# Kernel tuning notes

Measured on AMD Instinct MI355X. Metric: run time of the kernel, lower is better.

The kernel has to match this reference:

```python
import jax, jax.numpy as jnp
import numpy as np

N_HEAD = 16


def setup_inputs() -> dict:
    key = jax.random.key(0)
    k1, k2, k3 = jax.random.split(key, 3)
    B, T, C = 2, 2048, 1024
    x = jax.random.normal(k1, (B, T, C), dtype=jnp.float32)
    Wqkv = jax.random.normal(k2, (C, 3 * C), dtype=jnp.float32) * 0.02
    bqkv = jnp.zeros((3 * C,), dtype=jnp.float32)
    Wproj = jax.random.normal(k3, (C, C), dtype=jnp.float32) * 0.02
    bproj = jnp.zeros((C,), dtype=jnp.float32)
    return {"x": x, "Wqkv": Wqkv, "bqkv": bqkv, "Wproj": Wproj, "bproj": bproj}


def reference(x, Wqkv, bqkv, Wproj, bproj):
    b, t, c = x.shape
    h = N_HEAD
    d = c // h  # head_dim
    # qkv projection, split into q,k,v per head: (b,t,3,h,d)
    qkv = (x @ Wqkv + bqkv).reshape(b, t, 3, h, d)
    q, k, v = qkv[:, :, 0], qkv[:, :, 1], qkv[:, :, 2]  # each (b,t,h,d)
    # Faithful quirk of original: n_state = head_dim // heads, scale = 1/sqrt(n_state)
    scale = jnp.float32(1.0 / np.sqrt(d // h))
    # attn_mode == 'all': dense non-causal attention
    w = jnp.einsum('bqhd,bkhd->bhqk', q, k)  # (b,h,t,t)
    w = jax.nn.softmax(w * scale, axis=-1)
    a = jnp.einsum('bhqk,bkhd->bqhd', w, v).reshape(b, t, c)
    return a @ Wproj + bproj
```

## Files before the change

### kernel.cpp

```cpp
#include <hip/hip_runtime.h>

typedef float floatx4 __attribute__((ext_vector_type(4)));
typedef __bf16 bf16x8 __attribute__((ext_vector_type(8)));
typedef __bf16 bf16x4 __attribute__((ext_vector_type(4)));
typedef short short4v __attribute__((ext_vector_type(4)));

#define MFMA16 __builtin_amdgcn_mfma_f32_16x16x32_bf16

static __device__ __forceinline__ short4v b2s(bf16x4 x) {
  union { bf16x4 b; short4v s; } u; u.b = x; return u.s;
}
#define MFMAPV(a, b, c) \
  __builtin_amdgcn_mfma_f32_16x16x16bf16_1k(b2s(a), b2s(b), (c), 0, 0, 0)

typedef const __attribute__((address_space(1))) void* gas_t;
typedef __attribute__((address_space(3))) void* las_t;
#define GLD16(g, l) __builtin_amdgcn_global_load_lds((gas_t)(g), (las_t)(l), 16, 0, 0)

static __device__ __forceinline__ unsigned short f2bf(float f) {
  union { float f; unsigned int u; } v; v.f = f;
  unsigned int r = v.u + 0x7fffu + ((v.u >> 16) & 1u);
  return (unsigned short)(r >> 16);
}

static __device__ __forceinline__ void cast_transpose_tile(
    const float* __restrict__ in, unsigned short* __restrict__ out,
    int R, int C, int bx, int by) {
  const int r0 = by * 64, c0 = bx * 64;
  const int tid = threadIdx.x;
  __shared__ float tl[64][65];
  const int rr = tid >> 4, cc = (tid & 15) * 4;
#pragma unroll
  for (int i = 0; i < 4; ++i) {
    int row = rr + i * 16;
    float4 v = *(const float4*)(in + (size_t)(r0 + row) * C + c0 + cc);
    tl[row][cc] = v.x; tl[row][cc + 1] = v.y;
    tl[row][cc + 2] = v.z; tl[row][cc + 3] = v.w;
  }
  __syncthreads();
  const int cl = tid >> 2, rbase = (tid & 3) * 16;
  unsigned short o[16];
#pragma unroll
  for (int j = 0; j < 16; ++j) o[j] = f2bf(tl[rbase + j][cl]);
  unsigned short* dst = out + (size_t)(c0 + cl) * R + r0 + rbase;
  *(uint4*)dst = *(uint4*)o;
  *(uint4*)(dst + 8) = *(uint4*)(o + 8);
}

__global__ __launch_bounds__(256) void prologue_kernel(
    const float* __restrict__ x, unsigned short* __restrict__ Xb,
    const float* __restrict__ Wqkv, unsigned short* __restrict__ Wqkvt,
    const float* __restrict__ Wproj, unsigned short* __restrict__ Wprojt) {
  const int bid = blockIdx.x;
  if (bid < 4096) {
    int i = bid * 256 + threadIdx.x;
    float4 v = ((const float4*)x)[i];
    ushort4 o;
    o.x = f2bf(v.x); o.y = f2bf(v.y); o.z = f2bf(v.z); o.w = f2bf(v.w);
    ((ushort4*)Xb)[i] = o;
  } else if (bid < 4096 + 768) {
    int b2 = bid - 4096;
    cast_transpose_tile(Wqkv, Wqkvt, 1024, 3072, b2 % 48, b2 / 48);
  } else {
    int b3 = bid - 4096 - 768;
    cast_transpose_tile(Wproj, Wprojt, 1024, 1024, b3 % 16, b3 / 16);
  }
}

__global__ __launch_bounds__(256) void gemm_qkv(
    const unsigned short* __restrict__ A,
    const unsigned short* __restrict__ Bt,
    const float* __restrict__ bias,
    unsigned short* __restrict__ Q,
    unsigned short* __restrict__ Kc,
    unsigned short* __restrict__ Vt) {
  const int K = 1024;
  const int m0 = blockIdx.y * 128, n0 = blockIdx.x * 128;
  const int tid = threadIdx.x, w = tid >> 6, l = tid & 63;
  const int l16 = l & 15, lq = l >> 4;
  const int wm = w >> 1, wn = w & 1;
  const int which = n0 >> 10;

  __shared__ __align__(16) unsigned short SH[16384];
  unsigned short* As = SH;
  unsigned short* Bs = SH + 8192;

  floatx4 acc[4][4] = {};

  int sA[4], sB[4];
  unsigned ldso[4];
#pragma unroll
  for (int j = 0; j < 4; ++j) {
    int s = j * 256 + tid;
    int row = s >> 3, blk = (s & 7) ^ (row & 7);
    sA[j] = (m0 + row) * K + blk * 8;
    sB[j] = (n0 + row) * K + blk * 8;
    ldso[j] = (unsigned)(j * 256 + w * 64) * 8;
  }

  if (which == 2) {
    for (int k0 = 0; k0 < K; k0 += 64) {
      __syncthreads();
#pragma unroll
      for (int j = 0; j < 4; ++j) {
        GLD16(A + sA[j] + k0, As + ldso[j]);
        GLD16(Bt + sB[j] + k0, Bs + ldso[j]);
      }
      __syncthreads();
#pragma unroll
      for (int kk = 0; kk < 2; ++kk) {
        bf16x8 af[4], bf[4];
#pragma unroll
        for (int mi = 0; mi < 4; ++mi) {
          int row = wm * 64 + mi * 16 + l16;
          int blk = (kk * 4 + lq) ^ (l16 & 7);
          af[mi] = *(const bf16x8*)(As + row * 64 + blk * 8);
        }
#pragma unroll
        for (int ni = 0; ni < 4; ++ni) {
          int row = wn * 64 + ni * 16 + l16;
          int blk = (kk * 4 + lq) ^ (l16 & 7);
          bf[ni] = *(const bf16x8*)(Bs + row * 64 + blk * 8);
        }
#pragma unroll
        for (int ni = 0; ni < 4; ++ni)
#pragma unroll
          for (int mi = 0; mi < 4; ++mi)
            acc[mi][ni] = MFMA16(af[mi], bf[ni], acc[mi][ni], 0, 0, 0);
      }
    }
    float bv[4];
#pragma unroll
    for (int ni = 0; ni < 4; ++ni) bv[ni] = bias[n0 + wn * 64 + ni * 16 + l16];
    __syncthreads();
    unsigned short* E = SH + w * 2304;
    const int bh = (m0 >> 11) * 16 + ((n0 & 1023) >> 6) + wn;
    const int tt0 = (m0 & 2047) + wm * 64;
#pragma unroll
    for (int p = 0; p < 2; ++p) {
#pragma unroll
      for (int n2 = 0; n2 < 2; ++n2) {
        int ni = p * 2 + n2;
#pragma unroll
        for (int mi = 0; mi < 4; ++mi) {
          floatx4 vv = acc[mi][ni] + bv[ni];
          *(bf16x4*)(E + (n2 * 16 + l16) * 72 + mi * 16 + lq * 4) =
              __builtin_convertvector(vv, bf16x4);
        }
      }
#pragma unroll
      for (int s = 0; s < 4; ++s) {
        int dl = s * 8 + (l >> 3);
        bf16x8 vv = *(const bf16x8*)(E + dl * 72 + (l & 7) * 8);
        *(bf16x8*)(Vt + ((size_t)bh * 64 + p * 32 + dl) * 2048 + tt0 +
                   (l & 7) * 8) = vv;
      }
    }
  } else {
    for (int k0 = 0; k0 < K; k0 += 64) {
      __syncthreads();
#pragma unroll
      for (int j = 0; j < 4; ++j) {
        GLD16(A + sA[j] + k0, As + ldso[j]);
        GLD16(Bt + sB[j] + k0, Bs + ldso[j]);
      }
      __syncthreads();
#pragma unroll
      for (int kk = 0; kk < 2; ++kk) {
        bf16x8 af[4], bf[4];
#pragma unroll
        for (int mi = 0; mi < 4; ++mi) {
          int row = wm * 64 + mi * 16 + l16;
          int blk = (kk * 4 + lq) ^ (l16 & 7);
          af[mi] = *(const bf16x8*)(As + row * 64 + blk * 8);
        }
#pragma unroll
        for (int ni = 0; ni < 4; ++ni) {
          int row = wn * 64 + ni * 16 + l16;
          int blk = (kk * 4 + lq) ^ (l16 & 7);
          bf[ni] = *(const bf16x8*)(Bs + row * 64 + blk * 8);
        }
#pragma unroll
        for (int ni = 0; ni < 4; ++ni)
#pragma unroll
          for (int mi = 0; mi < 4; ++mi)
            acc[mi][ni] = MFMA16(bf[ni], af[mi], acc[mi][ni], 0, 0, 0);
      }
    }
    const float sc = (which == 0) ? 0.7213475204444817f : 1.0f;
    unsigned short* dst = (which == 0) ? Q : Kc;
    __syncthreads();
    unsigned short* E = SH + w * 2304;
    const int bh = (m0 >> 11) * 16 + ((n0 & 1023) >> 6) + wn;
    const size_t gbase = ((size_t)bh * 2048 + (m0 & 2047) + wm * 64) * 64;
#pragma unroll
    for (int p = 0; p < 2; ++p) {
#pragma unroll
      for (int m2 = 0; m2 < 2; ++m2) {
        int mi = p * 2 + m2;
#pragma unroll
        for (int ni = 0; ni < 4; ++ni) {
          int col0 = n0 + wn * 64 + ni * 16 + lq * 4;
          floatx4 bv = *(const floatx4*)(bias + col0);
          floatx4 vv = (acc[mi][ni] + bv) * sc;
          *(bf16x4*)(E + (m2 * 16 + l16) * 72 + ni * 16 + lq * 4) =
              __builtin_convertvector(vv, bf16x4);
        }
      }
#pragma unroll
      for (int s = 0; s < 4; ++s) {
        int rl = s * 8 + (l >> 3);
        bf16x8 vv = *(const bf16x8*)(E + rl * 72 + (l & 7) * 8);
        *(bf16x8*)(dst + gbase + (size_t)(p * 32 + rl) * 64 + (l & 7) * 8) =
            vv;
      }
    }
  }
}

__global__ __launch_bounds__(256, 2) void attn_kernel(
    const unsigned short* __restrict__ Q,
    const unsigned short* __restrict__ Kc,
    const unsigned short* __restrict__ Vt,
    unsigned short* __restrict__ AO) {
  const int T = 2048;
  const int bh = blockIdx.y, q0 = blockIdx.x * 128;
  const int tid = threadIdx.x, w = tid >> 6, l = tid & 63;
  const int l16 = l & 15, lq = l >> 4;
  const int kh = w >> 1, wq = w & 1;
  const int h128 = tid & 127;

  __shared__ __align__(16) unsigned short KVs[2][2][2][4096];
  __shared__ __align__(16) float Lred[512];

  bf16x8 qf[4][2];
  {
    const unsigned short* qb = Q + ((size_t)bh * T + q0 + wq * 64) * 64;
#pragma unroll
    for (int qs = 0; qs < 4; ++qs) {
      const unsigned short* qr = qb + (qs * 16 + l16) * 64;
      qf[qs][0] = *(const bf16x8*)(qr + lq * 8);
      qf[qs][1] = *(const bf16x8*)(qr + 32 + lq * 8);
    }
  }

  float l_lane[4] = {0.f, 0.f, 0.f, 0.f};
  floatx4 o_acc[4][4] = {};

  const unsigned short* kbase = Kc + (size_t)bh * T * 64;
  const unsigned short* vbase = Vt + (size_t)bh * 64 * T;
  int kro[4], vro[4];
  unsigned ldso[4];
#pragma unroll
  for (int j = 0; j < 4; ++j) {
    int s = j * 128 + h128;
    int row = s >> 3, blk = (s & 7) ^ (row & 7);
    kro[j] = row * 64 + blk * 8;
    vro[j] = row * T + blk * 8;
    ldso[j] = (unsigned)(j * 128 + wq * 64) * 8;
  }

  const int swz0 = (0 + lq) ^ (l16 & 7);
  const int swz1 = (4 + lq) ^ (l16 & 7);

  {
    int c0 = kh * 16;
#pragma unroll
    for (int j = 0; j < 4; ++j) {
      GLD16(kbase + c0 * 4096 + kro[j], &KVs[0][kh][0][ldso[j]]);
      GLD16(vbase + c0 * 64 + vro[j], &KVs[1][kh][0][ldso[j]]);
    }
  }

  for (int it = 0; it < 16; ++it) {
    __syncthreads();
    if (it + 1 < 16) {
      int cn = kh * 16 + it + 1, nb = (it + 1) & 1;
#pragma unroll
      for (int j = 0; j < 4; ++j) {
        GLD16(kbase + cn * 4096 + kro[j], &KVs[0][kh][nb][ldso[j]]);
        GLD16(vbase + cn * 64 + vro[j], &KVs[1][kh][nb][ldso[j]]);
      }
    }
    const unsigned short* kb = KVs[0][kh][it & 1];
    const unsigned short* vb = KVs[1][kh][it & 1];

    bf16x8 kf[4][2];
#pragma unroll
    for (int ct = 0; ct < 4; ++ct) {
      const unsigned short* kr = kb + (ct * 16 + l16) * 64;
      kf[ct][0] = *(const bf16x8*)(kr + swz0 * 8);
      kf[ct][1] = *(const bf16x8*)(kr + swz1 * 8);
    }

    bf16x4 pf[4][4];
#pragma unroll
    for (int qs = 0; qs < 4; ++qs) {
      floatx4 st[4];
#pragma unroll
      for (int ct = 0; ct < 4; ++ct) {
        floatx4 z = {};
        z = MFMA16(kf[ct][0], qf[qs][0], z, 0, 0, 0);
        z = MFMA16(kf[ct][1], qf[qs][1], z, 0, 0, 0);
        st[ct] = z;
      }
#pragma unroll
      for (int ct = 0; ct < 4; ++ct) {
        floatx4 pv;
        pv[0] = __builtin_amdgcn_exp2f(st[ct][0]);
        pv[1] = __builtin_amdgcn_exp2f(st[ct][1]);
        pv[2] = __builtin_amdgcn_exp2f(st[ct][2]);
        pv[3] = __builtin_amdgcn_exp2f(st[ct][3]);
        l_lane[qs] += (pv[0] + pv[1]) + (pv[2] + pv[3]);
        pf[qs][ct] = __builtin_convertvector(pv, bf16x4);
      }
    }

    const int vs = l16 & 7;
#pragma unroll
    for (int dt = 0; dt < 4; ++dt) {
      const unsigned short* vr = vb + (dt * 16 + l16) * 64 + (lq & 1) * 4;
      bf16x4 vf[4];
#pragma unroll
      for (int ct = 0; ct < 4; ++ct)
        vf[ct] = *(const bf16x4*)(vr + (((2 * ct + (lq >> 1)) ^ vs) << 3));
#pragma unroll
      for (int qs = 0; qs < 4; ++qs)
#pragma unroll
        for (int ct = 0; ct < 4; ++ct)
          o_acc[dt][qs] = MFMAPV(vf[ct], pf[qs][ct], o_acc[dt][qs]);
    }
  }

  __syncthreads();
  float* ex = (float*)&KVs[0][0][0][0];
  if (kh == 1) {
    float* r = ex + wq * 4096;
#pragma unroll
    for (int dt = 0; dt < 4; ++dt)
#pragma unroll
      for (int qs = 0; qs < 4; ++qs)
        *(floatx4*)(r + ((dt * 4 + qs) * 64 + l) * 4) = o_acc[dt][qs];
#pragma unroll
    for (int qs = 0; qs < 4; ++qs) Lred[(wq * 4 + qs) * 64 + l] = l_lane[qs];
  }
  __syncthreads();
  if (kh == 0) {
    const float* r = ex + wq * 4096;
    const int b = bh >> 4, h = bh & 15;
#pragma unroll
    for (int qs = 0; qs < 4; ++qs) {
      float ls = l_lane[qs] + Lred[(wq * 4 + qs) * 64 + l];
      ls += __shfl_xor(ls, 16, 64);
      ls += __shfl_xor(ls, 32, 64);
      float inv = 1.0f / ls;
      int t = q0 + wq * 64 + qs * 16 + l16;
#pragma unroll
      for (int dt = 0; dt < 4; ++dt) {
        floatx4 ov = o_acc[dt][qs] +
                     *(const floatx4*)(r + ((dt * 4 + qs) * 64 + l) * 4);
        ov *= inv;
        bf16x4 ob = __builtin_convertvector(ov, bf16x4);
        *(bf16x4*)(AO + ((size_t)b * 2048 + t) * 1024 + h * 64 + dt * 16 +
                   lq * 4) = ob;
      }
    }
  }
}

__global__ __launch_bounds__(256) void gemm_proj(
    const unsigned short* __restrict__ A,
    const unsigned short* __restrict__ Bt,
    const float* __restrict__ bias,
    float* __restrict__ out) {
  const int K = 1024, N = 1024;
  const int m0 = blockIdx.y * 128, n0 = blockIdx.x * 64;
  const int tid = threadIdx.x, w = tid >> 6, l = tid & 63;
  const int l16 = l & 15, lq = l >> 4;

  __shared__ __align__(16) unsigned short As[128 * 64];
  __shared__ __align__(16) unsigned short Bs[64 * 64];

  floatx4 acc[2][4] = {};

  int sA[4], sB[2];
  unsigned ldsoA[4], ldsoB[2];
#pragma unroll
  for (int j = 0; j < 4; ++j) {
    int s = j * 256 + tid;
    int row = s >> 3, blk = (s & 7) ^ (row & 7);
    sA[j] = (m0 + row) * K + blk * 8;
    ldsoA[j] = (unsigned)(j * 256 + w * 64) * 8;
  }
#pragma unroll
  for (int j = 0; j < 2; ++j) {
    int s = j * 256 + tid;
    int row = s >> 3, blk = (s & 7) ^ (row & 7);
    sB[j] = (n0 + row) * K + blk * 8;
    ldsoB[j] = (unsigned)(j * 256 + w * 64) * 8;
  }

  for (int k0 = 0; k0 < K; k0 += 64) {
    __syncthreads();
#pragma unroll
    for (int j = 0; j < 4; ++j) GLD16(A + sA[j] + k0, As + ldsoA[j]);
#pragma unroll
    for (int j = 0; j < 2; ++j) GLD16(Bt + sB[j] + k0, Bs + ldsoB[j]);
    __syncthreads();
#pragma unroll
    for (int kk = 0; kk < 2; ++kk) {
      bf16x8 af[2], bf[4];
#pragma unroll
      for (int mi = 0; mi < 2; ++mi) {
        int row = w * 32 + mi * 16 + l16;
        int blk = (kk * 4 + lq) ^ (l16 & 7);
        af[mi] = *(const bf16x8*)(As + row * 64 + blk * 8);
      }
#pragma unroll
      for (int ni = 0; ni < 4; ++ni) {
        int row = ni * 16 + l16;
        int blk = (kk * 4 + lq) ^ (l16 & 7);
        bf[ni] = *(const bf16x8*)(Bs + row * 64 + blk * 8);
      }
#pragma unroll
      for (int ni = 0; ni < 4; ++ni)
#pragma unroll
        for (int mi = 0; mi < 2; ++mi)
          acc[mi][ni] = MFMA16(bf[ni], af[mi], acc[mi][ni], 0, 0, 0);
    }
  }

#pragma unroll
  for (int mi = 0; mi < 2; ++mi) {
    int t = m0 + w * 32 + mi * 16 + l16;
#pragma unroll
    for (int ni = 0; ni < 4; ++ni) {
      int col0 = n0 + ni * 16 + lq * 4;
      floatx4 bv = *(const floatx4*)(bias + col0);
      *(floatx4*)(out + (size_t)t * N + col0) = acc[mi][ni] + bv;
    }
  }
}

extern "C" void kernel_launch(void* const* d_in, const int* in_sizes, int n_in,
                              void* d_out, int out_size, void* d_ws,
                              size_t ws_size, hipStream_t stream) {
  const float* x     = (const float*)d_in[0];
  const float* Wqkv  = (const float*)d_in[1];
  const float* bqkv  = (const float*)d_in[2];
  const float* Wproj = (const float*)d_in[3];
  const float* bproj = (const float*)d_in[4];
  float* out = (float*)d_out;

  unsigned short* Xb     = (unsigned short*)d_ws;
  unsigned short* Wqkvt  = Xb + 4194304;
  unsigned short* Wprojt = Wqkvt + 3145728;
  unsigned short* Qb     = Wprojt + 1048576;
  unsigned short* Kb     = Qb + 4194304;
  unsigned short* Vtb    = Kb + 4194304;
  unsigned short* AOb    = Vtb + 4194304;

  prologue_kernel<<<5120, 256, 0, stream>>>(x, Xb, Wqkv, Wqkvt, Wproj, Wprojt);
  gemm_qkv<<<dim3(24, 32), 256, 0, stream>>>(Xb, Wqkvt, bqkv, Qb, Kb, Vtb);
  attn_kernel<<<dim3(16, 32), 256, 0, stream>>>(Qb, Kb, Vtb, AOb);
  gemm_proj<<<dim3(16, 32), 256, 0, stream>>>(AOb, Wprojt, bproj, out);
}
```

Before: 184.9 us.

## Rewrite attention kernel with 32x32x16 MFMA and no intra-block KV split

The attention kernel now uses 32x32x16 bf16 MFMAs for both QK^T and PV. Each wave owns 32 query rows and walks all 32 key chunks, so the two-half KV split and its LDS reduction at the end are removed. The P fragments are repacked across lanes with xor-32 shuffles so they can feed the PV MFMA directly. The cost is more sequential iterations per block and fewer independent accumulators per wave, with shuffle overhead added inside the inner loop.

```diff
diff --git a/kernel.cpp b/kernel.cpp
--- a/kernel.cpp
+++ b/kernel.cpp
@@ -1,17 +1,14 @@
 #include <hip/hip_runtime.h>
 
 typedef float floatx4 __attribute__((ext_vector_type(4)));
+typedef float floatx16 __attribute__((ext_vector_type(16)));
 typedef __bf16 bf16x8 __attribute__((ext_vector_type(8)));
 typedef __bf16 bf16x4 __attribute__((ext_vector_type(4)));
-typedef short short4v __attribute__((ext_vector_type(4)));
+typedef __bf16 bf16x2 __attribute__((ext_vector_type(2)));
+typedef float floatx2 __attribute__((ext_vector_type(2)));
 
 #define MFMA16 __builtin_amdgcn_mfma_f32_16x16x32_bf16
-
-static __device__ __forceinline__ short4v b2s(bf16x4 x) {
-  union { bf16x4 b; short4v s; } u; u.b = x; return u.s;
-}
-#define MFMAPV(a, b, c) \
-  __builtin_amdgcn_mfma_f32_16x16x16bf16_1k(b2s(a), b2s(b), (c), 0, 0, 0)
+#define MFMA32 __builtin_amdgcn_mfma_f32_32x32x16_bf16
 
 typedef const __attribute__((address_space(1))) void* gas_t;
 typedef __attribute__((address_space(3))) void* las_t;
@@ -21,6 +18,13 @@
   union { float f; unsigned int u; } v; v.f = f;
   unsigned int r = v.u + 0x7fffu + ((v.u >> 16) & 1u);
   return (unsigned short)(r >> 16);
+}
+
+static __device__ __forceinline__ unsigned pk2(float a, float b) {
+  floatx2 v; v[0] = a; v[1] = b;
+  union { bf16x2 h; unsigned u; } u;
+  u.h = __builtin_convertvector(v, bf16x2);
+  return u.u;
 }
 
 static __device__ __forceinline__ void cast_transpose_tile(
@@ -226,146 +230,123 @@
   const int T = 2048;
   const int bh = blockIdx.y, q0 = blockIdx.x * 128;
   const int tid = threadIdx.x, w = tid >> 6, l = tid & 63;
-  const int l16 = l & 15, lq = l >> 4;
-  const int kh = w >> 1, wq = w & 1;
-  const int h128 = tid & 127;
-
-  __shared__ __align__(16) unsigned short KVs[2][2][2][4096];
-  __shared__ __align__(16) float Lred[512];
-
-  bf16x8 qf[4][2];
+  const int r31 = l & 31, g = l >> 5;
+
+  __shared__ __align__(16) unsigned short KVs[2][2][4096];
+
+  bf16x8 qf[4];
   {
-    const unsigned short* qb = Q + ((size_t)bh * T + q0 + wq * 64) * 64;
-#pragma unroll
-    for (int qs = 0; qs < 4; ++qs) {
-      const unsigned short* qr = qb + (qs * 16 + l16) * 64;
-      qf[qs][0] = *(const bf16x8*)(qr + lq * 8);
-      qf[qs][1] = *(const bf16x8*)(qr + 32 + lq * 8);
-    }
-  }
-
-  float l_lane[4] = {0.f, 0.f, 0.f, 0.f};
-  floatx4 o_acc[4][4] = {};
+    const unsigned short* qr =
+        Q + ((size_t)bh * T + q0 + w * 32 + r31) * 64 + g * 8;
+#pragma unroll
+    for (int ds = 0; ds < 4; ++ds) qf[ds] = *(const bf16x8*)(qr + ds * 16);
+  }
+
+  floatx16 o_acc[2] = {};
+  float l_lane = 0.f;
 
   const unsigned short* kbase = Kc + (size_t)bh * T * 64;
   const unsigned short* vbase = Vt + (size_t)bh * 64 * T;
-  int kro[4], vro[4];
-  unsigned ldso[4];
-#pragma unroll
-  for (int j = 0; j < 4; ++j) {
-    int s = j * 128 + h128;
+  int kro[2], vro[2];
+  unsigned ldso[2];
+#pragma unroll
+  for (int j = 0; j < 2; ++j) {
+    int s = j * 256 + tid;
     int row = s >> 3, blk = (s & 7) ^ (row & 7);
     kro[j] = row * 64 + blk * 8;
     vro[j] = row * T + blk * 8;
-    ldso[j] = (unsigned)(j * 128 + wq * 64) * 8;
-  }
-
-  const int swz0 = (0 + lq) ^ (l16 & 7);
-  const int swz1 = (4 + lq) ^ (l16 & 7);
-
-  {
-    int c0 = kh * 16;
-#pragma unroll
-    for (int j = 0; j < 4; ++j) {
-      GLD16(kbase + c0 * 4096 + kro[j], &KVs[0][kh][0][ldso[j]]);
-      GLD16(vbase + c0 * 64 + vro[j], &KVs[1][kh][0][ldso[j]]);
-    }
-  }
-
-  for (int it = 0; it < 16; ++it) {
+    ldso[j] = (unsigned)(j * 256 + (tid & 192)) * 8;
+  }
+
+#pragma unroll
+  for (int j = 0; j < 2; ++j) {
+    GLD16(kbase + kro[j], &KVs[0][0][ldso[j]]);
+    GLD16(vbase + vro[j], &KVs[0][1][ldso[j]]);
+  }
+
+  for (int c = 0; c < 32; ++c) {
     __syncthreads();
-    if (it + 1 < 16) {
-      int cn = kh * 16 + it + 1, nb = (it + 1) & 1;
-#pragma unroll
-      for (int j = 0; j < 4; ++j) {
-        GLD16(kbase + cn * 4096 + kro[j], &KVs[0][kh][nb][ldso[j]]);
-        GLD16(vbase + cn * 64 + vro[j], &KVs[1][kh][nb][ldso[j]]);
-      }
-    }
-    const unsigned short* kb = KVs[0][kh][it & 1];
-    const unsigned short* vb = KVs[1][kh][it & 1];
-
-    bf16x8 kf[4][2];
-#pragma unroll
-    for (int ct = 0; ct < 4; ++ct) {
-      const unsigned short* kr = kb + (ct * 16 + l16) * 64;
-      kf[ct][0] = *(const bf16x8*)(kr + swz0 * 8);
-      kf[ct][1] = *(const bf16x8*)(kr + swz1 * 8);
-    }
-
-    bf16x4 pf[4][4];
-#pragma unroll
-    for (int qs = 0; qs < 4; ++qs) {
-      floatx4 st[4];
-#pragma unroll
-      for (int ct = 0; ct < 4; ++ct) {
-        floatx4 z = {};
-        z = MFMA16(kf[ct][0], qf[qs][0], z, 0, 0, 0);
-        z = MFMA16(kf[ct][1], qf[qs][1], z, 0, 0, 0);
-        st[ct] = z;
-      }
-#pragma unroll
-      for (int ct = 0; ct < 4; ++ct) {
-        floatx4 pv;
-        pv[0] = __builtin_amdgcn_exp2f(st[ct][0]);
-        pv[1] = __builtin_amdgcn_exp2f(st[ct][1]);
-        pv[2] = __builtin_amdgcn_exp2f(st[ct][2]);
-        pv[3] = __builtin_amdgcn_exp2f(st[ct][3]);
-        l_lane[qs] += (pv[0] + pv[1]) + (pv[2] + pv[3]);
-        pf[qs][ct] = __builtin_convertvector(pv, bf16x4);
-      }
-    }
-
-    const int vs = l16 & 7;
-#pragma unroll
-    for (int dt = 0; dt < 4; ++dt) {
-      const unsigned short* vr = vb + (dt * 16 + l16) * 64 + (lq & 1) * 4;
-      bf16x4 vf[4];
-#pragma unroll
-      for (int ct = 0; ct < 4; ++ct)
-        vf[ct] = *(const bf16x4*)(vr + (((2 * ct + (lq >> 1)) ^ vs) << 3));
-#pragma unroll
-      for (int qs = 0; qs < 4; ++qs)
-#pragma unroll
-        for (int ct = 0; ct < 4; ++ct)
-          o_acc[dt][qs] = MFMAPV(vf[ct], pf[qs][ct], o_acc[dt][qs]);
-    }
-  }
-
-  __syncthreads();
-  float* ex = (float*)&KVs[0][0][0][0];
-  if (kh == 1) {
-    float* r = ex + wq * 4096;
-#pragma unroll
-    for (int dt = 0; dt < 4; ++dt)
-#pragma unroll
-      for (int qs = 0; qs < 4; ++qs)
-        *(floatx4*)(r + ((dt * 4 + qs) * 64 + l) * 4) = o_acc[dt][qs];
-#pragma unroll
-    for (int qs = 0; qs < 4; ++qs) Lred[(wq * 4 + qs) * 64 + l] = l_lane[qs];
-  }
-  __syncthreads();
-  if (kh == 0) {
-    const float* r = ex + wq * 4096;
-    const int b = bh >> 4, h = bh & 15;
-#pragma unroll
-    for (int qs = 0; qs < 4; ++qs) {
-      float ls = l_lane[qs] + Lred[(wq * 4 + qs) * 64 + l];
-      ls += __shfl_xor(ls, 16, 64);
-      ls += __shfl_xor(ls, 32, 64);
-      float inv = 1.0f / ls;
-      int t = q0 + wq * 64 + qs * 16 + l16;
-#pragma unroll
-      for (int dt = 0; dt < 4; ++dt) {
-        floatx4 ov = o_acc[dt][qs] +
-                     *(const floatx4*)(r + ((dt * 4 + qs) * 64 + l) * 4);
-        ov *= inv;
-        bf16x4 ob = __builtin_convertvector(ov, bf16x4);
-        *(bf16x4*)(AO + ((size_t)b * 2048 + t) * 1024 + h * 64 + dt * 16 +
-                   lq * 4) = ob;
-      }
-    }
-  }
+    if (c < 31) {
+      const int nb = (c + 1) & 1;
+#pragma unroll
+      for (int j = 0; j < 2; ++j) {
+        GLD16(kbase + (c + 1) * 4096 + kro[j], &KVs[nb][0][ldso[j]]);
+        GLD16(vbase + (c + 1) * 64 + vro[j], &KVs[nb][1][ldso[j]]);
+      }
+    }
+    const unsigned short* kb = KVs[c & 1][0];
+    const unsigned short* vb = KVs[c & 1][1];
+
+    floatx16 sac[2];
+#pragma unroll
+    for (int kt = 0; kt < 2; ++kt) {
+      const int row = kt * 32 + r31, rx = row & 7;
+      const unsigned short* kr = kb + row * 64;
+      floatx16 z = {};
+#pragma unroll
+      for (int ds = 0; ds < 4; ++ds)
+        z = MFMA32(*(const bf16x8*)(kr + ((ds * 2 + g) ^ rx) * 8), qf[ds], z,
+                   0, 0, 0);
+      sac[kt] = z;
+    }
+
+    bf16x8 pf[4];
+#pragma unroll
+    for (int kt = 0; kt < 2; ++kt) {
+      float p[16];
+#pragma unroll
+      for (int r = 0; r < 16; ++r) p[r] = __builtin_amdgcn_exp2f(sac[kt][r]);
+      l_lane += (((p[0] + p[1]) + (p[2] + p[3])) +
+                 ((p[4] + p[5]) + (p[6] + p[7]))) +
+                (((p[8] + p[9]) + (p[10] + p[11])) +
+                 ((p[12] + p[13]) + (p[14] + p[15])));
+#pragma unroll
+      for (int s2 = 0; s2 < 2; ++s2) {
+        unsigned cA = pk2(p[8 * s2 + 0], p[8 * s2 + 1]);
+        unsigned cB = pk2(p[8 * s2 + 2], p[8 * s2 + 3]);
+        unsigned cC = pk2(p[8 * s2 + 4], p[8 * s2 + 5]);
+        unsigned cD = pk2(p[8 * s2 + 6], p[8 * s2 + 7]);
+        unsigned xA = (unsigned)__shfl_xor((int)cA, 32, 64);
+        unsigned xB = (unsigned)__shfl_xor((int)cB, 32, 64);
+        unsigned xC = (unsigned)__shfl_xor((int)cC, 32, 64);
+        unsigned xD = (unsigned)__shfl_xor((int)cD, 32, 64);
+        union { unsigned u[4]; bf16x8 v; } pu;
+        pu.u[0] = g ? xC : cA;
+        pu.u[1] = g ? xD : cB;
+        pu.u[2] = g ? cC : xA;
+        pu.u[3] = g ? cD : xB;
+        pf[kt * 2 + s2] = pu.v;
+      }
+    }
+
+#pragma unroll
+    for (int dt = 0; dt < 2; ++dt) {
+      const int row = dt * 32 + r31, rx = row & 7;
+      const unsigned short* vr = vb + row * 64;
+#pragma unroll
+      for (int s = 0; s < 4; ++s) {
+        bf16x8 vf = *(const bf16x8*)(vr + ((s * 2 + g) ^ rx) * 8);
+        o_acc[dt] = MFMA32(vf, pf[s], o_acc[dt], 0, 0, 0);
+      }
+    }
+  }
+
+  float ls = l_lane + __shfl_xor(l_lane, 32, 64);
+  float inv = 1.0f / ls;
+  const int b = bh >> 4, h = bh & 15;
+  const int t = q0 + w * 32 + r31;
+  unsigned short* ao = AO + ((size_t)b * 2048 + t) * 1024 + h * 64;
+#pragma unroll
+  for (int dt = 0; dt < 2; ++dt)
+#pragma unroll
+    for (int rq = 0; rq < 4; ++rq) {
+      floatx4 ov;
+      ov[0] = o_acc[dt][rq * 4 + 0]; ov[1] = o_acc[dt][rq * 4 + 1];
+      ov[2] = o_acc[dt][rq * 4 + 2]; ov[3] = o_acc[dt][rq * 4 + 3];
+      ov *= inv;
+      *(bf16x4*)(ao + dt * 32 + rq * 8 + g * 4) =
+          __builtin_convertvector(ov, bf16x4);
+    }
 }
 
 __global__ __launch_bounds__(256) void gemm_proj(
```

After: 190.7 us. 1.03x slower.
